# Kernel optimization log

Measured on AMD Instinct MI355X. Metric: run time of the kernel, lower is better.

## Reference

```python
import jax, jax.numpy as jnp
import numpy as np

B, C = 2, 4
SPATIAL = (128, 128, 128)
N_PTS = 32          # num_points_per_class
THR = 0.5           # threshold


def setup_inputs() -> dict:
    key = jax.random.key(0)
    logits = jax.random.normal(key, (B, C) + SPATIAL, dtype=jnp.float32)
    return {"logits": logits}


def _extract_points(logits):
    """Vectorized equivalent of the per-(batch,class) nonzero/topk loop.

    For every (b, c): softmax prob > THR defines candidates; top-k by prob
    selects up to N_PTS points. Classes are visited in the original order
    (foreground 1..C-1, then background 0); valid points are compacted to
    the front per batch element; padding has label -1 and coords 0.
    Output width is fixed at C*N_PTS (jit-friendly) instead of the batch
    max count, but all valid (coord, label) entries and their order match.
    """
    b, c = logits.shape[:2]
    spatial = logits.shape[2:]
    dims = len(spatial)
    S = int(np.prod(spatial))
    probs = jax.nn.softmax(logits, axis=1).reshape(b, c, S)  # [b,c,S]
    # class visitation order: 1..C-1 then 0 (background last)
    order = jnp.concatenate([jnp.arange(1, c), jnp.arange(1)])  # [c]
    probs = probs[:, order]                                    # [b,c,S]
    score = jnp.where(probs > THR, probs, -jnp.inf)
    top_vals, top_idx = jax.lax.top_k(score, N_PTS)            # [b,c,N_PTS]
    valid = top_vals > -jnp.inf                                # [b,c,N_PTS]
    coords = jnp.stack(jnp.unravel_index(top_idx, spatial), axis=-1)  # [b,c,N_PTS,dims]
    labels = jnp.where(valid, order[None, :, None], -1)        # [b,c,N_PTS]
    coords = jnp.where(valid[..., None], coords, 0)
    # flatten classes and compact valid points to the front (stable sort)
    N = c * N_PTS
    labels = labels.reshape(b, N)
    coords = coords.reshape(b, N, dims)
    perm = jnp.argsort((labels < 0).astype(jnp.int32), axis=1, stable=True)  # [b,N]
    labels = jnp.take_along_axis(labels, perm, axis=1)
    coords = jnp.take_along_axis(coords, perm[..., None], axis=1)
    return coords.astype(jnp.int32), labels.astype(jnp.int32)


def reference(logits):
    coords, labels = _extract_points(logits)
    return coords, labels
```

## Files before the change

### kernel.cpp

```cpp
#include <hip/hip_runtime.h>
#include <stdint.h>

#define Bn 2
#define Cn 4
#define Sn (128 * 128 * 128)
#define NPTS 32
#define NBINS 1025
#define THRf 0.5f
#define PB 4096
#define BT 512
#define FCAP 2048

__device__ __forceinline__ int bin_of_bits(unsigned int u) {
    return (int)((u - 0x3F000000u) >> 13);
}

__device__ __forceinline__ void softmax_argmax4(float l0, float l1, float l2, float l3,
                                                int* cm_out, float* p_out) {
    float m = fmaxf(fmaxf(l0, l1), fmaxf(l2, l3));
    float e0 = expf(l0 - m);
    float e1 = expf(l1 - m);
    float e2 = expf(l2 - m);
    float e3 = expf(l3 - m);
    float s = ((e0 + e1) + e2) + e3;
    float em = e0; int cm = 0;
    if (e1 > em) { em = e1; cm = 1; }
    if (e2 > em) { em = e2; cm = 2; }
    if (e3 > em) { em = e3; cm = 3; }
    *cm_out = cm;
    *p_out = em / s;
}

__global__ __launch_bounds__(BT) void fused_kernel(const float* __restrict__ logits,
                                                   unsigned int* __restrict__ cnt,
                                                   uint2* __restrict__ cand,
                                                   int cap) {
    __shared__ unsigned int lh[Cn * NBINS];
    __shared__ unsigned int lcut[Cn], cls_cnt[Cn], cls_base[Cn], cls_pos[Cn];
    const int b = blockIdx.y;
    const int t = threadIdx.x;
    const int lane = t & 63;
    for (int j = t; j < Cn * NBINS; j += BT) lh[j] = 0u;
    if (t < Cn) { lcut[t] = 0u; cls_cnt[t] = 0u; cls_pos[t] = 0u; }
    __syncthreads();

    const float* base = logits + (size_t)b * Cn * Sn;
    const float4* s0 = (const float4*)base;
    const float4* s1 = (const float4*)(base + Sn);
    const float4* s2 = (const float4*)(base + 2 * Sn);
    const float4* s3 = (const float4*)(base + 3 * Sn);
    const int qs = blockIdx.x * (PB / 4);
    unsigned int pk[PB / BT];
    #pragma unroll
    for (int it = 0; it < PB / 4 / BT; ++it) {
        int q = qs + it * BT + t;
        float4 v0 = s0[q], v1 = s1[q], v2 = s2[q], v3 = s3[q];
        const float* a0 = &v0.x; const float* a1 = &v1.x;
        const float* a2 = &v2.x; const float* a3 = &v3.x;
        #pragma unroll
        for (int k = 0; k < 4; ++k) {
            int cm; float p;
            softmax_argmax4(a0[k], a1[k], a2[k], a3[k], &cm, &p);
            unsigned int pv = 0u;
            if (p > THRf) {
                unsigned int off = __float_as_uint(p) - 0x3F000000u;
                atomicAdd(&lh[cm * NBINS + (int)(off >> 13)], 1u);
                pv = (off << 2) | (unsigned int)cm;
            }
            pk[it * 4 + k] = pv;
        }
    }
    __syncthreads();

    {
        const int wave = t >> 6;
        if (wave < Cn) {
            const unsigned int* h = &lh[wave * NBINS];
            const int lo = lane * 17;
            unsigned int cs = 0;
            #pragma unroll
            for (int k = 0; k < 17; ++k) {
                int bin = lo + k;
                if (bin < NBINS) cs += h[bin];
            }
            unsigned int S = cs;
            #pragma unroll
            for (int off = 1; off < 64; off <<= 1) {
                unsigned int v = __shfl_down(S, off, 64);
                if (lane + off < 64) S += v;
            }
            unsigned int suf = S - cs;
            if (S >= NPTS && suf < NPTS) {
                unsigned int acc = suf;
                int hi = min(lo + 16, NBINS - 1);
                for (int bin = hi; bin >= lo; --bin) {
                    acc += h[bin];
                    if (acc >= NPTS) {
                        lcut[wave] = (unsigned int)bin;
                        cls_cnt[wave] = acc;
                        break;
                    }
                }
            }
            if (lane == 0 && S < NPTS) cls_cnt[wave] = S;
        }
    }
    __syncthreads();

    if (t < Cn && cls_cnt[t] > 0)
        cls_base[t] = atomicAdd(&cnt[b * Cn + t], cls_cnt[t]);
    __syncthreads();

    #pragma unroll
    for (int j = 0; j < PB / BT; ++j) {
        unsigned int pv = pk[j];
        if (pv != 0u) {
            unsigned int cm = pv & 3u;
            if ((pv >> 15) >= lcut[cm]) {
                unsigned int pos = cls_base[cm] + atomicAdd(&cls_pos[cm], 1u);
                if (pos < (unsigned int)cap) {
                    int it = j >> 2, k = j & 3;
                    unsigned int idx = (unsigned int)((qs + it * BT + t) * 4 + k);
                    cand[(size_t)(b * Cn + cm) * cap + pos] =
                        make_uint2(0x3F000000u + (pv >> 2), idx);
                }
            }
        }
    }
}

__global__ __launch_bounds__(1024) void select_emit(const unsigned int* __restrict__ cnt,
                                                    const uint2* __restrict__ cand,
                                                    int cap,
                                                    unsigned int* __restrict__ validn,
                                                    uint2* __restrict__ topk,
                                                    unsigned int* __restrict__ done,
                                                    int* __restrict__ out) {
    __shared__ unsigned int lh[NBINS];
    __shared__ uint2 fbuf[FCAP];
    __shared__ unsigned int s_m, s_T, s_old;
    const int bc = blockIdx.x, t = threadIdx.x;
    const int b = bc >> 2;
    const int n = min((int)cnt[bc], cap);
    for (int j = t; j < NBINS; j += 1024) lh[j] = 0u;
    if (t == 0) { s_m = 0u; s_T = 0u; }
    __syncthreads();
    const uint2* src = cand + (size_t)bc * cap;
    for (int j = t; j < n; j += 1024)
        atomicAdd(&lh[bin_of_bits(src[j].x)], 1u);
    __syncthreads();
    if (t < 64) {
        const int lane = t;
        const int lo = lane * 17;
        unsigned int cs = 0;
        #pragma unroll
        for (int k = 0; k < 17; ++k) {
            int bin = lo + k;
            if (bin < NBINS) cs += lh[bin];
        }
        unsigned int S = cs;
        #pragma unroll
        for (int off = 1; off < 64; off <<= 1) {
            unsigned int v = __shfl_down(S, off, 64);
            if (lane + off < 64) S += v;
        }
        unsigned int suf = S - cs;
        if (S >= NPTS && suf < NPTS) {
            unsigned int acc = suf;
            int hi = min(lo + 16, NBINS - 1);
            for (int bin = hi; bin >= lo; --bin) {
                acc += lh[bin];
                if (acc >= NPTS) { s_T = (unsigned int)bin; break; }
            }
        }
    }
    __syncthreads();
    const unsigned int T = s_T;
    for (int j = t; j < n; j += 1024) {
        uint2 e = src[j];
        if ((unsigned int)bin_of_bits(e.x) >= T) {
            unsigned int pos = atomicAdd(&s_m, 1u);
            if (pos < FCAP) fbuf[pos] = e;
        }
    }
    __syncthreads();
    const int m = min((int)s_m, FCAP);
    const int vn = min(n, NPTS);
    if (t == 0) validn[bc] = (unsigned int)vn;
    for (int i = t; i < m; i += 1024) {
        uint2 e = fbuf[i];
        int rank = 0;
        for (int j = 0; j < m; ++j) {
            uint2 o = fbuf[j];
            rank += (int)((o.x > e.x) || (o.x == e.x && o.y < e.y));
        }
        if (rank < vn) topk[bc * NPTS + rank] = e;
    }

    __threadfence();
    __syncthreads();
    if (t == 0) s_old = atomicAdd(&done[b], 1u);
    __syncthreads();
    if (s_old == 3u) {
        __threadfence();
        __shared__ int pre[Cn + 1];
        if (t == 0) {
            int acc = 0;
            for (int oc = 0; oc < Cn; ++oc) {
                pre[oc] = acc;
                acc += (int)validn[b * Cn + ((oc + 1) & 3)];
            }
            pre[Cn] = acc;
        }
        __syncthreads();
        if (t < Cn * NPTS) {
            const int j = t;
            int label = -1, z = 0, y = 0, x = 0;
            if (j < pre[Cn]) {
                int oc = 0;
                while (j >= pre[oc + 1]) ++oc;
                int c = (oc + 1) & 3;
                int r = j - pre[oc];
                uint2 e = topk[(b * Cn + c) * NPTS + r];
                int idx = (int)e.y;
                z = idx >> 14;
                y = (idx >> 7) & 127;
                x = idx & 127;
                label = c;
            }
            int* coords = out;
            int* labels = out + Bn * Cn * NPTS * 3;
            int bo = b * Cn * NPTS + j;
            coords[bo * 3 + 0] = z;
            coords[bo * 3 + 1] = y;
            coords[bo * 3 + 2] = x;
            labels[bo] = label;
        }
    }
}

extern "C" void kernel_launch(void* const* d_in, const int* in_sizes, int n_in,
                              void* d_out, int out_size, void* d_ws, size_t ws_size,
                              hipStream_t stream) {
    const float* logits = (const float*)d_in[0];
    int* out = (int*)d_out;

    unsigned int* cnt = (unsigned int*)d_ws;
    unsigned int* done = cnt + Bn * Cn;
    unsigned int* validn = done + Bn;
    uint2* topk = (uint2*)(validn + Bn * Cn);
    uint2* cand = topk + Bn * Cn * NPTS;
    size_t fixed = (size_t)((char*)cand - (char*)d_ws);
    int cap = (int)((ws_size - fixed) / (Bn * Cn * sizeof(uint2)));
    if (cap > (1 << 18)) cap = 1 << 18;
    if (cap < 4096) cap = 4096;

    hipMemsetAsync(cnt, 0, (Bn * Cn + Bn) * sizeof(unsigned int), stream);

    dim3 grid(Sn / PB, Bn);
    fused_kernel<<<grid, BT, 0, stream>>>(logits, cnt, cand, cap);
    select_emit<<<Bn * Cn, 1024, 0, stream>>>(cnt, cand, cap, validn, topk, done, out);
}
```

Before: 120.1 us.

## Replace global atomic candidate counters with per-block segments and drop memset

```diff
diff --git a/kernel.cpp b/kernel.cpp
--- a/kernel.cpp
+++ b/kernel.cpp
@@ -9,14 +9,16 @@
 #define THRf 0.5f
 #define PB 4096
 #define BT 512
+#define NBLK (Sn / PB)
+#define SEGCAP 128
 #define FCAP 2048
 
 __device__ __forceinline__ int bin_of_bits(unsigned int u) {
     return (int)((u - 0x3F000000u) >> 13);
 }
 
-__device__ __forceinline__ void softmax_argmax4(float l0, float l1, float l2, float l3,
-                                                int* cm_out, float* p_out) {
+__device__ __forceinline__ void softmax_parts4(float l0, float l1, float l2, float l3,
+                                               int* cm_out, float* em_out, float* s_out) {
     float m = fmaxf(fmaxf(l0, l1), fmaxf(l2, l3));
     float e0 = expf(l0 - m);
     float e1 = expf(l1 - m);
@@ -28,20 +30,22 @@
     if (e2 > em) { em = e2; cm = 2; }
     if (e3 > em) { em = e3; cm = 3; }
     *cm_out = cm;
-    *p_out = em / s;
+    *em_out = em;
+    *s_out = s;
 }
 
 __global__ __launch_bounds__(BT) void fused_kernel(const float* __restrict__ logits,
-                                                   unsigned int* __restrict__ cnt,
+                                                   unsigned int* __restrict__ cnt2,
                                                    uint2* __restrict__ cand,
-                                                   int cap) {
+                                                   unsigned int* __restrict__ done) {
     __shared__ unsigned int lh[Cn * NBINS];
-    __shared__ unsigned int lcut[Cn], cls_cnt[Cn], cls_base[Cn], cls_pos[Cn];
+    __shared__ unsigned int lcut[Cn], cls_cnt[Cn], cls_pos[Cn];
     const int b = blockIdx.y;
     const int t = threadIdx.x;
     const int lane = t & 63;
     for (int j = t; j < Cn * NBINS; j += BT) lh[j] = 0u;
     if (t < Cn) { lcut[t] = 0u; cls_cnt[t] = 0u; cls_pos[t] = 0u; }
+    if (blockIdx.x == 0 && b == 0 && t < Bn) done[t] = 0u;
     __syncthreads();
 
     const float* base = logits + (size_t)b * Cn * Sn;
@@ -59,13 +63,16 @@
         const float* a2 = &v2.x; const float* a3 = &v3.x;
         #pragma unroll
         for (int k = 0; k < 4; ++k) {
-            int cm; float p;
-            softmax_argmax4(a0[k], a1[k], a2[k], a3[k], &cm, &p);
+            int cm; float em, s;
+            softmax_parts4(a0[k], a1[k], a2[k], a3[k], &cm, &em, &s);
             unsigned int pv = 0u;
-            if (p > THRf) {
-                unsigned int off = __float_as_uint(p) - 0x3F000000u;
-                atomicAdd(&lh[cm * NBINS + (int)(off >> 13)], 1u);
-                pv = (off << 2) | (unsigned int)cm;
+            if (em > 0.5f * s) {
+                float p = em / s;
+                if (p > THRf) {
+                    unsigned int off = __float_as_uint(p) - 0x3F000000u;
+                    atomicAdd(&lh[cm * NBINS + (int)(off >> 13)], 1u);
+                    pv = (off << 2) | (unsigned int)cm;
+                }
             }
             pk[it * 4 + k] = pv;
         }
@@ -107,47 +114,53 @@
     }
     __syncthreads();
 
-    if (t < Cn && cls_cnt[t] > 0)
-        cls_base[t] = atomicAdd(&cnt[b * Cn + t], cls_cnt[t]);
-    __syncthreads();
-
     #pragma unroll
     for (int j = 0; j < PB / BT; ++j) {
         unsigned int pv = pk[j];
         if (pv != 0u) {
             unsigned int cm = pv & 3u;
             if ((pv >> 15) >= lcut[cm]) {
-                unsigned int pos = cls_base[cm] + atomicAdd(&cls_pos[cm], 1u);
-                if (pos < (unsigned int)cap) {
+                unsigned int pos = atomicAdd(&cls_pos[cm], 1u);
+                if (pos < SEGCAP) {
                     int it = j >> 2, k = j & 3;
                     unsigned int idx = (unsigned int)((qs + it * BT + t) * 4 + k);
-                    cand[(size_t)(b * Cn + cm) * cap + pos] =
+                    cand[((size_t)(b * Cn + cm) * NBLK + blockIdx.x) * SEGCAP + pos] =
                         make_uint2(0x3F000000u + (pv >> 2), idx);
                 }
             }
         }
     }
-}
-
-__global__ __launch_bounds__(1024) void select_emit(const unsigned int* __restrict__ cnt,
+    __syncthreads();
+    if (t < Cn)
+        cnt2[(size_t)(b * Cn + t) * NBLK + blockIdx.x] = min(cls_pos[t], (unsigned int)SEGCAP);
+}
+
+__global__ __launch_bounds__(1024) void select_emit(const unsigned int* __restrict__ cnt2,
                                                     const uint2* __restrict__ cand,
-                                                    int cap,
                                                     unsigned int* __restrict__ validn,
                                                     uint2* __restrict__ topk,
                                                     unsigned int* __restrict__ done,
                                                     int* __restrict__ out) {
     __shared__ unsigned int lh[NBINS];
+    __shared__ unsigned int scnt[NBLK];
     __shared__ uint2 fbuf[FCAP];
-    __shared__ unsigned int s_m, s_T, s_old;
+    __shared__ unsigned int s_n, s_m, s_T, s_old;
     const int bc = blockIdx.x, t = threadIdx.x;
     const int b = bc >> 2;
-    const int n = min((int)cnt[bc], cap);
     for (int j = t; j < NBINS; j += 1024) lh[j] = 0u;
-    if (t == 0) { s_m = 0u; s_T = 0u; }
-    __syncthreads();
-    const uint2* src = cand + (size_t)bc * cap;
-    for (int j = t; j < n; j += 1024)
-        atomicAdd(&lh[bin_of_bits(src[j].x)], 1u);
+    if (t == 0) { s_n = 0u; s_m = 0u; s_T = 0u; }
+    __syncthreads();
+    for (int j = t; j < NBLK; j += 1024) {
+        unsigned int c = cnt2[(size_t)bc * NBLK + j];
+        scnt[j] = c;
+        if (c) atomicAdd(&s_n, c);
+    }
+    __syncthreads();
+    const uint2* seg = cand + (size_t)bc * NBLK * SEGCAP;
+    for (int j = t; j < NBLK * SEGCAP; j += 1024) {
+        if ((unsigned int)(j & (SEGCAP - 1)) < scnt[j >> 7])
+            atomicAdd(&lh[bin_of_bits(seg[j].x)], 1u);
+    }
     __syncthreads();
     if (t < 64) {
         const int lane = t;
@@ -176,16 +189,18 @@
     }
     __syncthreads();
     const unsigned int T = s_T;
-    for (int j = t; j < n; j += 1024) {
-        uint2 e = src[j];
-        if ((unsigned int)bin_of_bits(e.x) >= T) {
-            unsigned int pos = atomicAdd(&s_m, 1u);
-            if (pos < FCAP) fbuf[pos] = e;
+    for (int j = t; j < NBLK * SEGCAP; j += 1024) {
+        if ((unsigned int)(j & (SEGCAP - 1)) < scnt[j >> 7]) {
+            uint2 e = seg[j];
+            if ((unsigned int)bin_of_bits(e.x) >= T) {
+                unsigned int pos = atomicAdd(&s_m, 1u);
+                if (pos < FCAP) fbuf[pos] = e;
+            }
         }
     }
     __syncthreads();
     const int m = min((int)s_m, FCAP);
-    const int vn = min(n, NPTS);
+    const int vn = min((int)s_n, NPTS);
     if (t == 0) validn[bc] = (unsigned int)vn;
     for (int i = t; i < m; i += 1024) {
         uint2 e = fbuf[i];
@@ -245,19 +260,13 @@
     const float* logits = (const float*)d_in[0];
     int* out = (int*)d_out;
 
-    unsigned int* cnt = (unsigned int*)d_ws;
-    unsigned int* done = cnt + Bn * Cn;
-    unsigned int* validn = done + Bn;
-    uint2* topk = (uint2*)(validn + Bn * Cn);
+    unsigned int* cnt2 = (unsigned int*)d_ws;
+    unsigned int* validn = cnt2 + Bn * Cn * NBLK;
+    unsigned int* done = validn + Bn * Cn;
+    uint2* topk = (uint2*)(done + Bn + 6);
     uint2* cand = topk + Bn * Cn * NPTS;
-    size_t fixed = (size_t)((char*)cand - (char*)d_ws);
-    int cap = (int)((ws_size - fixed) / (Bn * Cn * sizeof(uint2)));
-    if (cap > (1 << 18)) cap = 1 << 18;
-    if (cap < 4096) cap = 4096;
-
-    hipMemsetAsync(cnt, 0, (Bn * Cn + Bn) * sizeof(unsigned int), stream);
-
-    dim3 grid(Sn / PB, Bn);
-    fused_kernel<<<grid, BT, 0, stream>>>(logits, cnt, cand, cap);
-    select_emit<<<Bn * Cn, 1024, 0, stream>>>(cnt, cand, cap, validn, topk, done, out);
-}
+
+    dim3 grid(NBLK, Bn);
+    fused_kernel<<<grid, BT, 0, stream>>>(logits, cnt2, cand, done);
+    select_emit<<<Bn * Cn, 1024, 0, stream>>>(cnt2, cand, validn, topk, done, out);
+}
```

New measurement: 139.9 us. 1.16x slower.
